# Kernel optimization log

Hardware: AMD Instinct MI355X
Metric: run time of the kernel (lower is better)

The kernel has to match this reference:

```python
import jax, jax.numpy as jnp
import numpy as np

N = 50000          # nodes
E = 800000         # edges (before self loops)
F_IN = 16
HID = 64
HEADS = 4
C = 64             # per-head out channels (concat=False)
G = 64             # graphs in batch
NEG_SLOPE = 0.2


def setup_inputs() -> dict:
    key = jax.random.key(0)
    ks = jax.random.split(key, 20)
    inp = {
        "x": jax.random.normal(ks[0], (N, F_IN), jnp.float32),
        "edge_index": jax.random.randint(ks[1], (2, E), 0, N, jnp.int64),
        "batch": jnp.sort(jax.random.randint(ks[2], (N,), 0, G, jnp.int64)),
        "W_in": jax.random.normal(ks[3], (HID, F_IN), jnp.float32) * 0.1,
        "b_in": jnp.zeros((HID,), jnp.float32),
        "W_out": jax.random.normal(ks[4], (1, HID), jnp.float32) * 0.1,
        "b_out": jnp.zeros((1,), jnp.float32),
    }
    for l in range(3):
        inp[f"W{l}"] = jax.random.normal(ks[5 + 4 * l], (HEADS * C, HID), jnp.float32) * 0.1
        inp[f"asrc{l}"] = jax.random.normal(ks[6 + 4 * l], (HEADS, C), jnp.float32) * 0.1
        inp[f"adst{l}"] = jax.random.normal(ks[7 + 4 * l], (HEADS, C), jnp.float32) * 0.1
        inp[f"bg{l}"] = jnp.zeros((HID,), jnp.float32)
    return inp


def _gat_layer(x, W, a_src, a_dst, bias, src, dst, n):
    # x: [N, HID] -> h: [N, HEADS, C]
    h = (x @ W.T).reshape(n, HEADS, C)
    alpha_s = jnp.einsum("nhc,hc->nh", h, a_src)   # [N, H]
    alpha_d = jnp.einsum("nhc,hc->nh", h, a_dst)
    e = jax.nn.leaky_relu(alpha_s[src] + alpha_d[dst], NEG_SLOPE)  # [E', H]
    # segment softmax over incoming edges of each dst node
    m = jax.ops.segment_max(e, dst, num_segments=n)
    e = jnp.exp(e - m[dst])
    s = jax.ops.segment_sum(e, dst, num_segments=n)
    alpha = e / (s[dst] + 1e-16)                                   # [E', H]
    msg = alpha[:, :, None] * h[src]                               # [E', H, C]
    out = jax.ops.segment_sum(msg, dst, num_segments=n)            # [N, H, C]
    return out.mean(axis=1) + bias                                 # concat=False: head mean


def reference(x, W_in, b_in, W0, asrc0, adst0, bg0, W1, asrc1, adst1, bg1,
              W2, asrc2, adst2, bg2, W_out, b_out, edge_index, batch):
    n = x.shape[0]
    # add self loops (PyG GATConv default)
    loops = jnp.arange(n, dtype=edge_index.dtype)
    src = jnp.concatenate([edge_index[0], loops])
    dst = jnp.concatenate([edge_index[1], loops])

    h = x @ W_in.T + b_in
    for W, a_s, a_d, bg in ((W0, asrc0, adst0, bg0),
                            (W1, asrc1, adst1, bg1),
                            (W2, asrc2, adst2, bg2)):
        h = jax.nn.relu(_gat_layer(h, W, a_s, a_d, bg, src, dst, n))
        # dropout p=0.2 is inactive in eval mode

    # global mean pool over graphs
    sums = jax.ops.segment_sum(h, batch, num_segments=G)
    cnt = jax.ops.segment_sum(jnp.ones((n,), h.dtype), batch, num_segments=G)
    graph_emb = sums / jnp.maximum(cnt, 1.0)[:, None]              # [G, HID]

    return jax.nn.sigmoid(graph_emb @ W_out.T + b_out)             # [G, 1]
```

## Files before the change

### kernel.cpp

```cpp
#include <hip/hip_runtime.h>
#include <hip/hip_bf16.h>
#include <hip/hip_fp16.h>

#define HID 64
#define HEADS 4
#define GCNT 64
#define F_IN 16
#define NEG 0.2f
#define NBUCK 256
#define BSLOT 6144
#define SCHUNK 2048

typedef _Float16 f16x8 __attribute__((ext_vector_type(8)));
typedef float f32x4 __attribute__((ext_vector_type(4)));

__device__ __forceinline__ unsigned pack_h2(float a, float b) {
  __half2 h = __floats2half2_rn(a, b);
  union { __half2 h; unsigned u; } c;
  c.h = h;
  return c.u;
}
__device__ __forceinline__ __half2 uas_h2(unsigned u) {
  union { unsigned u; __half2 h; } c;
  c.u = u;
  return c.h;
}
__device__ __forceinline__ unsigned h2_as_u(__half2 h) {
  union { __half2 h; unsigned u; } c;
  c.h = h;
  return c.u;
}
__device__ __forceinline__ __half2 xor16_add(__half2 v) {
  unsigned u = (unsigned)__shfl_xor((int)h2_as_u(v), 16, 64);
  return __hadd2(v, uas_h2(u));
}

__global__ __launch_bounds__(256) void k_pre(
    const float* __restrict__ W0, const float* __restrict__ asrc,
    const float* __restrict__ adst, const float* __restrict__ Win,
    const float* __restrict__ bin, int* __restrict__ bcur,
    float* __restrict__ vb, float* __restrict__ c8) {
  int t = threadIdx.x;
  if (blockIdx.x == 0) {
    bcur[t] = 0;
    return;
  }
  __shared__ float vaL[512];
#pragma unroll
  for (int it = 0; it < 2; ++it) {
    int idx = t + it * 256;
    int q = idx >> 6, j = idx & 63;
    const float* a = (q < 4) ? asrc : adst;
    int h = q & 3;
    float s = 0.f;
    for (int c = 0; c < 64; ++c) s += a[h * 64 + c] * W0[(h * 64 + c) * 64 + j];
    vaL[idx] = s;
  }
  __syncthreads();
  if (t < 128) {
    int q = t >> 4, k = t & 15;
    float s = 0.f;
    for (int j = 0; j < 64; ++j) s += vaL[q * 64 + j] * Win[j * F_IN + k];
    vb[t] = s;
  } else if (t < 136) {
    int q = t - 128;
    float s = 0.f;
    for (int j = 0; j < 64; ++j) s += vaL[q * 64 + j] * bin[j];
    c8[q] = s;
  }
}

__global__ __launch_bounds__(256) void k_bucket(
    const int* __restrict__ ei, int* __restrict__ bcur,
    unsigned* __restrict__ tmp, int E, int N) {
  __shared__ int hist[NBUCK];
  __shared__ int base[NBUCK];
  int t = threadIdx.x;
  int start = blockIdx.x * SCHUNK;
  int end = min(start + SCHUNK, E + N);
  hist[t] = 0;
  __syncthreads();
  unsigned val[8];
  int rank[8];
  bool ok[8];
#pragma unroll
  for (int k = 0; k < 8; ++k) {
    int i = start + t + k * 256;
    ok[k] = i < end;
    if (ok[k]) {
      int s, d;
      if (i < E) {
        s = ei[i];
        d = ei[E + i];
      } else {
        s = d = i - E;
      }
      val[k] = ((unsigned)d << 16) | (unsigned)s;
      rank[k] = atomicAdd(&hist[d >> 8], 1);
    }
  }
  __syncthreads();
  int h = hist[t];
  base[t] = h ? atomicAdd(&bcur[t], h) : 0;
  __syncthreads();
#pragma unroll
  for (int k = 0; k < 8; ++k) {
    if (ok[k]) {
      int bk = (int)(val[k] >> 24);
      int idx = base[bk] + rank[k];
      if (idx < BSLOT) tmp[(size_t)bk * BSLOT + idx] = val[k];
    }
  }
}

__global__ __launch_bounds__(256) void k_bsort(
    const unsigned* __restrict__ tmp, const int* __restrict__ bcur,
    int* __restrict__ rowptr, int* __restrict__ col, int N) {
  __shared__ int s[NBUCK];
  __shared__ int hist[NBUCK];
  __shared__ int pref[NBUCK];
  int b = blockIdx.x, t = threadIdx.x;
  int c = min(bcur[t], BSLOT);
  s[t] = c;
  __syncthreads();
  for (int o = 1; o < 256; o <<= 1) {
    int x = (t >= o) ? s[t - o] : 0;
    __syncthreads();
    s[t] += x;
    __syncthreads();
  }
  int base = (b == 0) ? 0 : s[b - 1];
  int total = s[255];
  int cntb = min(bcur[b], BSLOT);
  hist[t] = 0;
  __syncthreads();
  for (int j = t; j < cntb; j += 256)
    atomicAdd(&hist[(tmp[(size_t)b * BSLOT + j] >> 16) & 255], 1);
  __syncthreads();
  int v = hist[t];
  pref[t] = v;
  __syncthreads();
  for (int o = 1; o < 256; o <<= 1) {
    int x = (t >= o) ? pref[t - o] : 0;
    __syncthreads();
    pref[t] += x;
    __syncthreads();
  }
  pref[t] -= v;
  __syncthreads();
  int node = b * 256 + t;
  if (node < N) rowptr[node] = base + pref[t];
  if (b == 255 && t == 255) rowptr[N] = total;
  hist[t] = 0;
  __syncthreads();
  for (int j = t; j < cntb; j += 256) {
    unsigned e = tmp[(size_t)b * BSLOT + j];
    int d8 = (int)((e >> 16) & 255);
    int r = atomicAdd(&hist[d8], 1);
    col[base + pref[d8] + r] = (int)(e & 0xffffu);
  }
}

__global__ void k_init(const float* __restrict__ x, const float* __restrict__ Win,
                       const float* __restrict__ bin,
                       const float* __restrict__ W0, const float* __restrict__ W1,
                       const float* __restrict__ W2,
                       __half* __restrict__ Wh3, __half* __restrict__ Wcat3,
                       float* __restrict__ sums, const float* __restrict__ vb,
                       const float* __restrict__ c8,
                       float* __restrict__ as_, float* __restrict__ ad_,
                       __half* __restrict__ hh, int N) {
  int b = blockIdx.x, t = threadIdx.x;
  if (b < 384) {
    int i = b * 256 + t;
    if (i < 49152) {
      const float* W = (i < 16384) ? W0 : (i < 32768) ? W1 : W2;
      Wh3[i] = __float2half(W[i & 16383]);
    } else {
      int j = i - 49152;
      int l = j >> 14;
      int r = j & 16383;
      int c = r >> 8;
      int k256 = r & 255;
      int h = k256 & 3, kk = k256 >> 2;
      const float* W = (l == 0) ? W0 : (l == 1) ? W1 : W2;
      Wcat3[j] = __float2half(0.25f * W[(h * 64 + c) * 64 + kk]);
    }
    return;
  }
  if (b < 401) {
    int i = (b - 384) * 256 + t;
    if (i < GCNT * HID + GCNT) sums[i] = 0.f;
    return;
  }
  int i = (b - 401) * 256 + t;
  if (i >= N * HID) return;
  int n = i >> 6, j = i & 63;
  const float* xr = x + (size_t)n * F_IN;
  const float* wr = Win + j * F_IN;
  float xv[F_IN];
  float acc = bin[j];
#pragma unroll
  for (int k = 0; k < F_IN; ++k) {
    xv[k] = xr[k];
    acc = fmaf(xv[k], wr[k], acc);
  }
  hh[i] = __float2half(acc);
  if (j < 8) {
    const float* vbq = vb + j * 16;
    float s = c8[j];
#pragma unroll
    for (int k = 0; k < F_IN; ++k) s = fmaf(xv[k], vbq[k], s);
    if (j < 4) as_[(size_t)n * 4 + j] = s;
    else ad_[(size_t)n * 4 + (j - 4)] = s;
  }
}

__device__ __forceinline__ void gat_one_node(
    int node, int lane, const __half* __restrict__ h, const float* __restrict__ as_,
    const float* __restrict__ ad_, const int* __restrict__ rowptr,
    const int* __restrict__ col, __half* __restrict__ Mrow) {
  int r0 = rowptr[node];
  int deg = rowptr[node + 1] - r0;
  float4 adv = *(const float4*)(ad_ + (size_t)node * 4);

  if (deg <= 64) {
    int off = 0;
    float x0 = 0.f, x1 = 0.f, x2 = 0.f, x3 = 0.f;
    if (lane < deg) {
      int s = col[r0 + lane];
      off = s << 6;
      float4 av = *(const float4*)(as_ + (size_t)s * 4);
      float e0 = av.x + adv.x; e0 = (e0 > 0.f) ? e0 : NEG * e0;
      float e1 = av.y + adv.y; e1 = (e1 > 0.f) ? e1 : NEG * e1;
      float e2 = av.z + adv.z; e2 = (e2 > 0.f) ? e2 : NEG * e2;
      float e3 = av.w + adv.w; e3 = (e3 > 0.f) ? e3 : NEG * e3;
      x0 = __expf(fminf(e0, 60.f));
      x1 = __expf(fminf(e1, 60.f));
      x2 = __expf(fminf(e2, 60.f));
      x3 = __expf(fminf(e3, 60.f));
    }
    float s0 = x0, s1 = x1, s2 = x2, s3 = x3;
#pragma unroll
    for (int o = 32; o; o >>= 1) {
      s0 += __shfl_xor(s0, o, 64);
      s1 += __shfl_xor(s1, o, 64);
      s2 += __shfl_xor(s2, o, 64);
      s3 += __shfl_xor(s3, o, 64);
    }
    unsigned w01 = pack_h2(x0 / (s0 + 1e-16f), x1 / (s1 + 1e-16f));
    unsigned w23 = pack_h2(x2 / (s2 + 1e-16f), x3 / (s3 + 1e-16f));
    __half2 acc01 = __floats2half2_rn(0.f, 0.f);
    __half2 acc23 = acc01;
#pragma unroll 4
    for (int j = 0; j < deg; ++j) {
      int oj = __builtin_amdgcn_readlane(off, j) + lane;
      unsigned W01 = __builtin_amdgcn_readlane(w01, j);
      unsigned W23 = __builtin_amdgcn_readlane(w23, j);
      __half2 hv = __half2half2(h[oj]);
      acc01 = __hfma2(hv, uas_h2(W01), acc01);
      acc23 = __hfma2(hv, uas_h2(W23), acc23);
    }
    *(__half2*)&Mrow[lane * 4] = acc01;
    *(__half2*)&Mrow[lane * 4 + 2] = acc23;
    return;
  }
  float m0 = -1e30f, m1 = -1e30f, m2 = -1e30f, m3 = -1e30f;
  for (int j = lane; j < deg; j += 64) {
    int s = col[r0 + j];
    float4 av = *(const float4*)(as_ + (size_t)s * 4);
    float e0 = av.x + adv.x; e0 = (e0 > 0.f) ? e0 : NEG * e0; m0 = fmaxf(m0, e0);
    float e1 = av.y + adv.y; e1 = (e1 > 0.f) ? e1 : NEG * e1; m1 = fmaxf(m1, e1);
    float e2 = av.z + adv.z; e2 = (e2 > 0.f) ? e2 : NEG * e2; m2 = fmaxf(m2, e2);
    float e3 = av.w + adv.w; e3 = (e3 > 0.f) ? e3 : NEG * e3; m3 = fmaxf(m3, e3);
  }
#pragma unroll
  for (int o = 32; o; o >>= 1) {
    m0 = fmaxf(m0, __shfl_xor(m0, o, 64));
    m1 = fmaxf(m1, __shfl_xor(m1, o, 64));
    m2 = fmaxf(m2, __shfl_xor(m2, o, 64));
    m3 = fmaxf(m3, __shfl_xor(m3, o, 64));
  }
  float s0 = 0.f, s1 = 0.f, s2 = 0.f, s3 = 0.f;
  for (int j = lane; j < deg; j += 64) {
    int s = col[r0 + j];
    float4 av = *(const float4*)(as_ + (size_t)s * 4);
    float e0 = av.x + adv.x; e0 = (e0 > 0.f) ? e0 : NEG * e0; s0 += __expf(e0 - m0);
    float e1 = av.y + adv.y; e1 = (e1 > 0.f) ? e1 : NEG * e1; s1 += __expf(e1 - m1);
    float e2 = av.z + adv.z; e2 = (e2 > 0.f) ? e2 : NEG * e2; s2 += __expf(e2 - m2);
    float e3 = av.w + adv.w; e3 = (e3 > 0.f) ? e3 : NEG * e3; s3 += __expf(e3 - m3);
  }
#pragma unroll
  for (int o = 32; o; o >>= 1) {
    s0 += __shfl_xor(s0, o, 64);
    s1 += __shfl_xor(s1, o, 64);
    s2 += __shfl_xor(s2, o, 64);
    s3 += __shfl_xor(s3, o, 64);
  }
  float i0 = 1.f / (s0 + 1e-16f), i1 = 1.f / (s1 + 1e-16f);
  float i2 = 1.f / (s2 + 1e-16f), i3 = 1.f / (s3 + 1e-16f);
  float a0 = 0.f, a1 = 0.f, a2 = 0.f, a3 = 0.f;
  for (int j = 0; j < deg; ++j) {
    int s = col[r0 + j];
    float4 av = *(const float4*)(as_ + (size_t)s * 4);
    float e0 = av.x + adv.x; e0 = (e0 > 0.f) ? e0 : NEG * e0;
    float e1 = av.y + adv.y; e1 = (e1 > 0.f) ? e1 : NEG * e1;
    float e2 = av.z + adv.z; e2 = (e2 > 0.f) ? e2 : NEG * e2;
    float e3 = av.w + adv.w; e3 = (e3 > 0.f) ? e3 : NEG * e3;
    float hv = __half2float(h[(s << 6) + lane]);
    a0 = fmaf(__expf(e0 - m0) * i0, hv, a0);
    a1 = fmaf(__expf(e1 - m1) * i1, hv, a1);
    a2 = fmaf(__expf(e2 - m2) * i2, hv, a2);
    a3 = fmaf(__expf(e3 - m3) * i3, hv, a3);
  }
  *(__half2*)&Mrow[lane * 4] = __floats2half2_rn(a0, a1);
  *(__half2*)&Mrow[lane * 4 + 2] = __floats2half2_rn(a2, a3);
}

__device__ __forceinline__ void gat_pair(
    int pr, int lane, int half, int l5, int N,
    const __half* __restrict__ h, const float* __restrict__ as_,
    const float* __restrict__ ad_, const int* __restrict__ rowptr,
    const int* __restrict__ col, __half* __restrict__ Mt) {
  int n0 = pr * 2;
  int n1 = min(n0 + 1, N - 1);
  int mynode = half ? n1 : n0;
  int r0 = rowptr[mynode];
  int dg = rowptr[mynode + 1] - r0;
  int dgA = __builtin_amdgcn_readlane(dg, 0);
  int dgB = __builtin_amdgcn_readlane(dg, 32);

  if (dgA <= 32 && dgB <= 32) {
    float4 adv = *(const float4*)(ad_ + (size_t)mynode * 4);
    int off = 0;
    float x0 = 0.f, x1 = 0.f, x2 = 0.f, x3 = 0.f;
    if (l5 < dg) {
      int s = col[r0 + l5];
      off = s << 6;
      float4 av = *(const float4*)(as_ + (size_t)s * 4);
      float e0 = av.x + adv.x; e0 = (e0 > 0.f) ? e0 : NEG * e0;
      float e1 = av.y + adv.y; e1 = (e1 > 0.f) ? e1 : NEG * e1;
      float e2 = av.z + adv.z; e2 = (e2 > 0.f) ? e2 : NEG * e2;
      float e3 = av.w + adv.w; e3 = (e3 > 0.f) ? e3 : NEG * e3;
      x0 = __expf(fminf(e0, 60.f));
      x1 = __expf(fminf(e1, 60.f));
      x2 = __expf(fminf(e2, 60.f));
      x3 = __expf(fminf(e3, 60.f));
    }
    float s0 = x0, s1 = x1, s2 = x2, s3 = x3;
#pragma unroll
    for (int o = 16; o; o >>= 1) {
      s0 += __shfl_xor(s0, o, 64);
      s1 += __shfl_xor(s1, o, 64);
      s2 += __shfl_xor(s2, o, 64);
      s3 += __shfl_xor(s3, o, 64);
    }
    unsigned w01 = pack_h2(x0 / (s0 + 1e-16f), x1 / (s1 + 1e-16f));
    unsigned w23 = pack_h2(x2 / (s2 + 1e-16f), x3 / (s3 + 1e-16f));

    int g = l5 >> 4, li = l5 & 15;
    const uint2* h4p = (const uint2*)h;
    __half2 z = __floats2half2_rn(0.f, 0.f);
    __half2 a0_01 = z, a0_23 = z, a1_01 = z, a1_23 = z;
    __half2 a2_01 = z, a2_23 = z, a3_01 = z, a3_23 = z;
    int mdeg = max(dgA, dgB);
    int baddr = half << 7;
#pragma unroll 2
    for (int j = 0; j < mdeg; j += 2) {
      int addr = baddr + (j + g) * 4;
      int oj = __builtin_amdgcn_ds_bpermute(addr, off);
      unsigned W01 = (unsigned)__builtin_amdgcn_ds_bpermute(addr, (int)w01);
      unsigned W23 = (unsigned)__builtin_amdgcn_ds_bpermute(addr, (int)w23);
      uint2 hv = h4p[(oj >> 2) + li];
      __half2 ha = uas_h2(hv.x), hb = uas_h2(hv.y);
      __half2 wA = uas_h2(W01), wB = uas_h2(W23);
      __half2 c0 = __low2half2(ha), c1 = __high2half2(ha);
      __half2 c2 = __low2half2(hb), c3 = __high2half2(hb);
      a0_01 = __hfma2(c0, wA, a0_01); a0_23 = __hfma2(c0, wB, a0_23);
      a1_01 = __hfma2(c1, wA, a1_01); a1_23 = __hfma2(c1, wB, a1_23);
      a2_01 = __hfma2(c2, wA, a2_01); a2_23 = __hfma2(c2, wB, a2_23);
      a3_01 = __hfma2(c3, wA, a3_01); a3_23 = __hfma2(c3, wB, a3_23);
    }
    a0_01 = xor16_add(a0_01); a0_23 = xor16_add(a0_23);
    a1_01 = xor16_add(a1_01); a1_23 = xor16_add(a1_23);
    a2_01 = xor16_add(a2_01); a2_23 = xor16_add(a2_23);
    a3_01 = xor16_add(a3_01); a3_23 = xor16_add(a3_23);
    if (g == 0) {
      __half* row = &Mt[(mynode & 15) * 264 + li * 16];
      uint4 st1, st2;
      st1.x = h2_as_u(a0_01); st1.y = h2_as_u(a0_23);
      st1.z = h2_as_u(a1_01); st1.w = h2_as_u(a1_23);
      st2.x = h2_as_u(a2_01); st2.y = h2_as_u(a2_23);
      st2.z = h2_as_u(a3_01); st2.w = h2_as_u(a3_23);
      *(uint4*)&row[0] = st1;
      *(uint4*)&row[8] = st2;
    }
  } else {
    gat_one_node(n0, lane, h, as_, ad_, rowptr, col, &Mt[(n0 & 15) * 264]);
    if (n1 != n0) gat_one_node(n1, lane, h, as_, ad_, rowptr, col, &Mt[(n1 & 15) * 264]);
  }
}

template <bool FIN>
__global__ __launch_bounds__(256) void k_gatf(
    const __half* __restrict__ h, const float* __restrict__ as_,
    const float* __restrict__ ad_, const int* __restrict__ rowptr,
    const int* __restrict__ col, const __half* __restrict__ Wcat,
    const float* __restrict__ bg, const __half* __restrict__ Wn,
    const float* __restrict__ asrc, const float* __restrict__ adst,
    __half* __restrict__ hout, float* __restrict__ nas, float* __restrict__ nad,
    const int* __restrict__ batchv, float* __restrict__ gsums,
    int N) {
  __shared__ __half Mt[16 * 264];
  __shared__ __half O[16 * 72];
  int tid = threadIdx.x;
  int lane = tid & 63, wv = tid >> 6;
  int tile = blockIdx.x;
  int half = lane >> 5, l5 = lane & 31;
  int npairs = (N + 1) >> 1;

  int pr0 = tile * 8 + wv * 2;
  int pr1 = pr0 + 1;
  bool has0 = pr0 < npairs, has1 = pr1 < npairs;
  if (has0 && has1) {
    int my0 = min(pr0 * 2 + half, N - 1);
    int my1 = min(pr1 * 2 + half, N - 1);
    int r0a = rowptr[my0];
    int dga = rowptr[my0 + 1] - r0a;
    int r0b = rowptr[my1];
    int dgb = rowptr[my1 + 1] - r0b;
    int dA0 = __builtin_amdgcn_readlane(dga, 0);
    int dB0 = __builtin_amdgcn_readlane(dga, 32);
    int dA1 = __builtin_amdgcn_readlane(dgb, 0);
    int dB1 = __builtin_amdgcn_readlane(dgb, 32);

    if (dA0 <= 32 && dB0 <= 32 && dA1 <= 32 && dB1 <= 32) {
      float4 adva = *(const float4*)(ad_ + (size_t)my0 * 4);
      float4 advb = *(const float4*)(ad_ + (size_t)my1 * 4);
      int offa = 0, offb = 0;
      float xa0 = 0.f, xa1 = 0.f, xa2 = 0.f, xa3 = 0.f;
      float xb0 = 0.f, xb1 = 0.f, xb2 = 0.f, xb3 = 0.f;
      if (l5 < dga) {
        int s = col[r0a + l5];
        offa = s << 6;
        float4 av = *(const float4*)(as_ + (size_t)s * 4);
        float e0 = av.x + adva.x; e0 = (e0 > 0.f) ? e0 : NEG * e0;
        float e1 = av.y + adva.y; e1 = (e1 > 0.f) ? e1 : NEG * e1;
        float e2 = av.z + adva.z; e2 = (e2 > 0.f) ? e2 : NEG * e2;
        float e3 = av.w + adva.w; e3 = (e3 > 0.f) ? e3 : NEG * e3;
        xa0 = __expf(fminf(e0, 60.f));
        xa1 = __expf(fminf(e1, 60.f));
        xa2 = __expf(fminf(e2, 60.f));
        xa3 = __expf(fminf(e3, 60.f));
      }
      if (l5 < dgb) {
        int s = col[r0b + l5];
        offb = s << 6;
        float4 av = *(const float4*)(as_ + (size_t)s * 4);
        float e0 = av.x + advb.x; e0 = (e0 > 0.f) ? e0 : NEG * e0;
        float e1 = av.y + advb.y; e1 = (e1 > 0.f) ? e1 : NEG * e1;
        float e2 = av.z + advb.z; e2 = (e2 > 0.f) ? e2 : NEG * e2;
        float e3 = av.w + advb.w; e3 = (e3 > 0.f) ? e3 : NEG * e3;
        xb0 = __expf(fminf(e0, 60.f));
        xb1 = __expf(fminf(e1, 60.f));
        xb2 = __expf(fminf(e2, 60.f));
        xb3 = __expf(fminf(e3, 60.f));
      }
      float sa0 = xa0, sa1 = xa1, sa2 = xa2, sa3 = xa3;
      float sb0 = xb0, sb1 = xb1, sb2 = xb2, sb3 = xb3;
#pragma unroll
      for (int o = 16; o; o >>= 1) {
        sa0 += __shfl_xor(sa0, o, 64);
        sa1 += __shfl_xor(sa1, o, 64);
        sa2 += __shfl_xor(sa2, o, 64);
        sa3 += __shfl_xor(sa3, o, 64);
        sb0 += __shfl_xor(sb0, o, 64);
        sb1 += __shfl_xor(sb1, o, 64);
        sb2 += __shfl_xor(sb2, o, 64);
        sb3 += __shfl_xor(sb3, o, 64);
      }
      unsigned w01a = pack_h2(xa0 / (sa0 + 1e-16f), xa1 / (sa1 + 1e-16f));
      unsigned w23a = pack_h2(xa2 / (sa2 + 1e-16f), xa3 / (sa3 + 1e-16f));
      unsigned w01b = pack_h2(xb0 / (sb0 + 1e-16f), xb1 / (sb1 + 1e-16f));
      unsigned w23b = pack_h2(xb2 / (sb2 + 1e-16f), xb3 / (sb3 + 1e-16f));

      uint4* EB = (uint4*)&Mt[wv * 1056];
      EB[half * 32 + l5] = make_uint4((unsigned)offa, w01a, w23a, 0u);
      EB[64 + half * 32 + l5] = make_uint4((unsigned)offb, w01b, w23b, 0u);

      int g = l5 >> 4, li = l5 & 15;
      const uint2* h4p = (const uint2*)h;
      __half2 z = __floats2half2_rn(0.f, 0.f);
      __half2 pa0 = z, pa1 = z, pa2 = z, pa3 = z, pa4 = z, pa5 = z, pa6 = z, pa7 = z;
      __half2 pb0 = z, pb1 = z, pb2 = z, pb3 = z, pb4 = z, pb5 = z, pb6 = z, pb7 = z;
      int mm = max(max(dA0, dB0), max(dA1, dB1));
      int ebase = half * 32;
#pragma unroll 2
      for (int j = 0; j < mm; j += 2) {
        uint4 ra = EB[ebase + j + g];
        uint4 rb = EB[64 + ebase + j + g];
        uint2 hva = h4p[((int)ra.x >> 2) + li];
        uint2 hvb = h4p[((int)rb.x >> 2) + li];
        {
          __half2 ha = uas_h2(hva.x), hb = uas_h2(hva.y);
          __half2 wA = uas_h2(ra.y), wB = uas_h2(ra.z);
          __half2 c0 = __low2half2(ha), c1 = __high2half2(ha);
          __half2 c2 = __low2half2(hb), c3 = __high2half2(hb);
          pa0 = __hfma2(c0, wA, pa0); pa1 = __hfma2(c0, wB, pa1);
          pa2 = __hfma2(c1, wA, pa2); pa3 = __hfma2(c1, wB, pa3);
          pa4 = __hfma2(c2, wA, pa4); pa5 = __hfma2(c2, wB, pa5);
          pa6 = __hfma2(c3, wA, pa6); pa7 = __hfma2(c3, wB, pa7);
        }
        {
          __half2 ha = uas_h2(hvb.x), hb = uas_h2(hvb.y);
          __half2 wA = uas_h2(rb.y), wB = uas_h2(rb.z);
          __half2 c0 = __low2half2(ha), c1 = __high2half2(ha);
          __half2 c2 = __low2half2(hb), c3 = __high2half2(hb);
          pb0 = __hfma2(c0, wA, pb0); pb1 = __hfma2(c0, wB, pb1);
          pb2 = __hfma2(c1, wA, pb2); pb3 = __hfma2(c1, wB, pb3);
          pb4 = __hfma2(c2, wA, pb4); pb5 = __hfma2(c2, wB, pb5);
          pb6 = __hfma2(c3, wA, pb6); pb7 = __hfma2(c3, wB, pb7);
        }
      }
      pa0 = xor16_add(pa0); pa1 = xor16_add(pa1); pa2 = xor16_add(pa2); pa3 = xor16_add(pa3);
      pa4 = xor16_add(pa4); pa5 = xor16_add(pa5); pa6 = xor16_add(pa6); pa7 = xor16_add(pa7);
      pb0 = xor16_add(pb0); pb1 = xor16_add(pb1); pb2 = xor16_add(pb2); pb3 = xor16_add(pb3);
      pb4 = xor16_add(pb4); pb5 = xor16_add(pb5); pb6 = xor16_add(pb6); pb7 = xor16_add(pb7);
      if (g == 0) {
        __half* rowA = &Mt[(my0 & 15) * 264 + li * 16];
        __half* rowB = &Mt[(my1 & 15) * 264 + li * 16];
        uint4 s1, s2;
        s1.x = h2_as_u(pa0); s1.y = h2_as_u(pa1); s1.z = h2_as_u(pa2); s1.w = h2_as_u(pa3);
        s2.x = h2_as_u(pa4); s2.y = h2_as_u(pa5); s2.z = h2_as_u(pa6); s2.w = h2_as_u(pa7);
        *(uint4*)&rowA[0] = s1;
        *(uint4*)&rowA[8] = s2;
        s1.x = h2_as_u(pb0); s1.y = h2_as_u(pb1); s1.z = h2_as_u(pb2); s1.w = h2_as_u(pb3);
        s2.x = h2_as_u(pb4); s2.y = h2_as_u(pb5); s2.z = h2_as_u(pb6); s2.w = h2_as_u(pb7);
        *(uint4*)&rowB[0] = s1;
        *(uint4*)&rowB[8] = s2;
      }
    } else {
      gat_pair(pr0, lane, half, l5, N, h, as_, ad_, rowptr, col, Mt);
      gat_pair(pr1, lane, half, l5, N, h, as_, ad_, rowptr, col, Mt);
    }
  } else if (has0) {
    gat_pair(pr0, lane, half, l5, N, h, as_, ad_, rowptr, col, Mt);
  }
  __syncthreads();

  int quad = lane >> 4, n16 = lane & 15;
  const f16x8* WC = (const f16x8*)Wcat;
  int ch1 = wv * 16 + n16;
  float bias1 = bg[ch1];
  f32x4 c1 = {0.f, 0.f, 0.f, 0.f};
#pragma unroll
  for (int i = 0; i < 8; ++i) {
    f16x8 a = *(const f16x8*)&Mt[n16 * 264 + (i * 4 + quad) * 8];
    c1 = __builtin_amdgcn_mfma_f32_16x16x32_f16(a, WC[ch1 * 32 + i * 4 + quad], c1, 0, 0, 0);
  }
#pragma unroll
  for (int r = 0; r < 4; ++r) {
    float v = fmaxf(c1[r] + bias1, 0.f);
    O[(quad * 4 + r) * 72 + ch1] = __float2half(v);
  }
  __syncthreads();

  if (FIN) {
    if (tid < 64) {
      float* cnt_ = gsums + GCNT * HID;
      int c = tid;
      int nmax = min(16, N - tile * 16);
      int curg = -1;
      float acc = 0.f;
      int cacc = 0;
      for (int i = 0; i < nmax; ++i) {
        int gph = batchv[tile * 16 + i];
        float v = __half2float(O[i * 72 + c]);
        if (gph != curg) {
          if (curg >= 0) {
            atomicAdd(&gsums[curg * HID + c], acc);
            if (c == 0) atomicAdd(&cnt_[curg], (float)cacc);
          }
          curg = gph;
          acc = 0.f;
          cacc = 0;
        }
        acc += v;
        ++cacc;
      }
      if (curg >= 0) {
        atomicAdd(&gsums[curg * HID + c], acc);
        if (c == 0) atomicAdd(&cnt_[curg], (float)cacc);
      }
    }
    return;
  }

  {
    int nd = tid >> 4, c0 = (tid & 15) * 4;
    int node = tile * 16 + nd;
    if (node < N) {
      uint2 v = *(const uint2*)&O[nd * 72 + c0];
      *(uint2*)&hout[(size_t)node * 64 + c0] = v;
    }
  }
  {
    const f16x8* WN = (const f16x8*)Wn;
    f16x8 a0 = *(const f16x8*)&O[n16 * 72 + quad * 8];
    f16x8 a1 = *(const f16x8*)&O[n16 * 72 + 32 + quad * 8];
    f32x4 accs[4];
#pragma unroll
    for (int nt = 0; nt < 4; ++nt) {
      int ch = wv * 64 + nt * 16 + n16;
      f32x4 zz = {0.f, 0.f, 0.f, 0.f};
      zz = __builtin_amdgcn_mfma_f32_16x16x32_f16(a0, WN[ch * 8 + quad], zz, 0, 0, 0);
      zz = __builtin_amdgcn_mfma_f32_16x16x32_f16(a1, WN[ch * 8 + 4 + quad], zz, 0, 0, 0);
      accs[nt] = zz;
    }
#pragma unroll
    for (int r = 0; r < 4; ++r) {
      float vs = 0.f, vd = 0.f;
#pragma unroll
      for (int nt = 0; nt < 4; ++nt) {
        int ch = wv * 64 + nt * 16 + n16;
        vs = fmaf(accs[nt][r], asrc[ch], vs);
        vd = fmaf(accs[nt][r], adst[ch], vd);
      }
#pragma unroll
      for (int o = 8; o; o >>= 1) {
        vs += __shfl_xor(vs, o, 64);
        vd += __shfl_xor(vd, o, 64);
      }
      int node = tile * 16 + quad * 4 + r;
      if (n16 == 0 && node < N) {
        nas[(size_t)node * 4 + wv] = vs;
        nad[(size_t)node * 4 + wv] = vd;
      }
    }
  }
}

__global__ void k_out(const float* __restrict__ sums, const float* __restrict__ cnt,
                      const float* __restrict__ Wout, const float* __restrict__ bout,
                      float* __restrict__ out) {
  int g = blockIdx.x, lane = threadIdx.x;
  float cg = fmaxf(cnt[g], 1.f);
  float v = (sums[g * HID + lane] / cg) * Wout[lane];
#pragma unroll
  for (int o = 32; o; o >>= 1) v += __shfl_xor(v, o, 64);
  if (lane == 0) out[g] = 1.f / (1.f + __expf(-v));
}

extern "C" void kernel_launch(void* const* d_in, const int* in_sizes, int n_in,
                              void* d_out, int out_size, void* d_ws, size_t ws_size,
                              hipStream_t stream) {
  const float* x    = (const float*)d_in[0];
  const int*   ei   = (const int*)d_in[1];
  const int*   batch= (const int*)d_in[2];
  const float* Win  = (const float*)d_in[3];
  const float* bin  = (const float*)d_in[4];
  const float* Wout = (const float*)d_in[5];
  const float* bout = (const float*)d_in[6];
  const float* Wl[3]    = {(const float*)d_in[7],  (const float*)d_in[11], (const float*)d_in[15]};
  const float* asrcl[3] = {(const float*)d_in[8],  (const float*)d_in[12], (const float*)d_in[16]};
  const float* adstl[3] = {(const float*)d_in[9],  (const float*)d_in[13], (const float*)d_in[17]};
  const float* bgl[3]   = {(const float*)d_in[10], (const float*)d_in[14], (const float*)d_in[18]};

  int N = in_sizes[2];
  int E = in_sizes[1] / 2;
  int EE = E + N;

  char* p = (char*)d_ws;
  auto alloc = [&](size_t bytes) {
    char* r = p;
    p += (bytes + 255) & ~(size_t)255;
    return r;
  };
  int*      rowptr = (int*)alloc((size_t)(N + 1) * 4);
  int*      col    = (int*)alloc((size_t)EE * 4);
  unsigned* tmp    = (unsigned*)alloc((size_t)NBUCK * BSLOT * 4);
  int*      bcur   = (int*)alloc(NBUCK * 4);
  float*    vb     = (float*)alloc(128 * 4);
  float*    c8     = (float*)alloc(8 * 4);
  __half*   hhA    = (__half*)alloc((size_t)N * HID * 2);
  __half*   hhB    = (__half*)alloc((size_t)N * HID * 2);
  float*    asA    = (float*)alloc((size_t)N * HEADS * 4);
  float*    adA    = (float*)alloc((size_t)N * HEADS * 4);
  float*    asB    = (float*)alloc((size_t)N * HEADS * 4);
  float*    adB    = (float*)alloc((size_t)N * HEADS * 4);
  __half*   Wh3    = (__half*)alloc(3 * 16384 * 2);
  __half*   Wcat3  = (__half*)alloc(3 * 16384 * 2);
  float*    sums   = (float*)alloc((size_t)(GCNT * HID + GCNT) * 4);
  float*    cnt    = sums + GCNT * HID;

  int tiles = (N + 15) / 16;

  k_pre<<<2, 256, 0, stream>>>(Wl[0], asrcl[0], adstl[0], Win, bin, bcur, vb, c8);
  k_bucket<<<(EE + SCHUNK - 1) / SCHUNK, 256, 0, stream>>>(ei, bcur, tmp, E, N);
  k_bsort<<<NBUCK, 256, 0, stream>>>(tmp, bcur, rowptr, col, N);

  k_init<<<401 + (N * HID + 255) / 256, 256, 0, stream>>>(
      x, Win, bin, Wl[0], Wl[1], Wl[2], Wh3, Wcat3, sums, vb, c8, asA, adA, hhA, N);

  k_gatf<false><<<tiles, 256, 0, stream>>>(hhA, asA, adA, rowptr, col,
                                           Wcat3, bgl[0], Wh3 + 16384, asrcl[1], adstl[1],
                                           hhB, asB, adB, nullptr, nullptr, N);
  k_gatf<false><<<tiles, 256, 0, stream>>>(hhB, asB, adB, rowptr, col,
                                           Wcat3 + 16384, bgl[1], Wh3 + 32768, asrcl[2], adstl[2],
                                           hhA, asA, adA, nullptr, nullptr, N);
  k_gatf<true><<<tiles, 256, 0, stream>>>(hhA, asA, adA, rowptr, col,
                                          Wcat3 + 32768, bgl[2], nullptr, nullptr, nullptr,
                                          nullptr, nullptr, nullptr, batch, sums, N);

  k_out<<<GCNT, 64, 0, stream>>>(sums, cnt, Wout, bout, (float*)d_out);
}
```

Before: 314.6 us.

## Split fused GAT layer into gather and GEMM kernels, merge bucket with init

Each fused GAT layer kernel is split in two. A gather/softmax kernel writes the aggregated per-node messages to a global buffer M, and a separate MFMA GEMM kernel reads M back. M shares workspace with the bucket temp buffer. The bucketing kernel and the init kernel are also merged into one launch to cut launch count. The split frees shared memory in the gather kernel, which may raise occupancy, but it adds a global round trip of about 25 MB of f16 per layer and three more launches.

Measured after the change: 365.4 us. 1.16x slower.

```diff
diff --git a/kernel.cpp b/kernel.cpp
--- a/kernel.cpp
+++ b/kernel.cpp
@@ -70,46 +70,102 @@
   }
 }
 
-__global__ __launch_bounds__(256) void k_bucket(
+__global__ __launch_bounds__(256) void k_binit(
     const int* __restrict__ ei, int* __restrict__ bcur,
-    unsigned* __restrict__ tmp, int E, int N) {
-  __shared__ int hist[NBUCK];
-  __shared__ int base[NBUCK];
+    unsigned* __restrict__ tmp, int E, int N,
+    const float* __restrict__ x, const float* __restrict__ Win,
+    const float* __restrict__ bin,
+    const float* __restrict__ W0, const float* __restrict__ W1,
+    const float* __restrict__ W2,
+    __half* __restrict__ Wh3, __half* __restrict__ Wcat3,
+    float* __restrict__ sums, const float* __restrict__ vb,
+    const float* __restrict__ c8,
+    float* __restrict__ as_, float* __restrict__ ad_,
+    __half* __restrict__ hh, int BUK) {
   int t = threadIdx.x;
-  int start = blockIdx.x * SCHUNK;
-  int end = min(start + SCHUNK, E + N);
-  hist[t] = 0;
-  __syncthreads();
-  unsigned val[8];
-  int rank[8];
-  bool ok[8];
-#pragma unroll
-  for (int k = 0; k < 8; ++k) {
-    int i = start + t + k * 256;
-    ok[k] = i < end;
-    if (ok[k]) {
-      int s, d;
-      if (i < E) {
-        s = ei[i];
-        d = ei[E + i];
-      } else {
-        s = d = i - E;
-      }
-      val[k] = ((unsigned)d << 16) | (unsigned)s;
-      rank[k] = atomicAdd(&hist[d >> 8], 1);
-    }
-  }
-  __syncthreads();
-  int h = hist[t];
-  base[t] = h ? atomicAdd(&bcur[t], h) : 0;
-  __syncthreads();
-#pragma unroll
-  for (int k = 0; k < 8; ++k) {
-    if (ok[k]) {
-      int bk = (int)(val[k] >> 24);
-      int idx = base[bk] + rank[k];
-      if (idx < BSLOT) tmp[(size_t)bk * BSLOT + idx] = val[k];
-    }
+  if (blockIdx.x < BUK) {
+    __shared__ int hist[NBUCK];
+    __shared__ int base[NBUCK];
+    int start = blockIdx.x * SCHUNK;
+    int end = min(start + SCHUNK, E + N);
+    hist[t] = 0;
+    __syncthreads();
+    unsigned val[8];
+    int rank[8];
+    bool ok[8];
+#pragma unroll
+    for (int k = 0; k < 8; ++k) {
+      int i = start + t + k * 256;
+      ok[k] = i < end;
+      if (ok[k]) {
+        int s, d;
+        if (i < E) {
+          s = ei[i];
+          d = ei[E + i];
+        } else {
+          s = d = i - E;
+        }
+        val[k] = ((unsigned)d << 16) | (unsigned)s;
+        rank[k] = atomicAdd(&hist[d >> 8], 1);
+      }
+    }
+    __syncthreads();
+    int h = hist[t];
+    base[t] = h ? atomicAdd(&bcur[t], h) : 0;
+    __syncthreads();
+#pragma unroll
+    for (int k = 0; k < 8; ++k) {
+      if (ok[k]) {
+        int bk = (int)(val[k] >> 24);
+        int idx = base[bk] + rank[k];
+        if (idx < BSLOT) tmp[(size_t)bk * BSLOT + idx] = val[k];
+      }
+    }
+    return;
+  }
+  int b = blockIdx.x - BUK;
+  if (b < 384) {
+    int i = b * 256 + t;
+    if (i < 49152) {
+      const float* W = (i < 16384) ? W0 : (i < 32768) ? W1 : W2;
+      Wh3[i] = __float2half(W[i & 16383]);
+    } else {
+      int j = i - 49152;
+      int l = j >> 14;
+      int r = j & 16383;
+      int c = r >> 8;
+      int k256 = r & 255;
+      int h = k256 & 3, kk = k256 >> 2;
+      const float* W = (l == 0) ? W0 : (l == 1) ? W1 : W2;
+      Wcat3[j] = __float2half(0.25f * W[(h * 64 + c) * 64 + kk]);
+    }
+    return;
+  }
+  if (b < 401) {
+    int i = (b - 384) * 256 + t;
+    if (i < GCNT * HID + GCNT) sums[i] = 0.f;
+    return;
+  }
+  int i = (b - 401) * 256 + t;
+  if (i >= N * HID) return;
+  int n = i >> 6, j = i & 63;
+  const float* xr = x + (size_t)n * F_IN;
+  const float* wr = Win + j * F_IN;
+  float xv[F_IN];
+  float acc = bin[j];
+#pragma unroll
+  for (int k = 0; k < F_IN; ++k) {
+    xv[k] = xr[k];
+    acc = fmaf(xv[k], wr[k], acc);
+  }
+  hh[i] = __float2half(acc);
+  if (j < 8) {
+    const float* vbq = vb + j * 16;
+    float s = c8[j];
+#pragma unroll
+    for (int k = 0; k < F_IN; ++k) s = fmaf(xv[k], vbq[k], s);
+    if (j < 4) as_[(size_t)n * 4 + j] = s;
+    else ad_[(size_t)n * 4 + (j - 4)] = s;
   }
 }
 
@@ -161,61 +217,6 @@
   }
 }
 
-__global__ void k_init(const float* __restrict__ x, const float* __restrict__ Win,
-                       const float* __restrict__ bin,
-                       const float* __restrict__ W0, const float* __restrict__ W1,
-                       const float* __restrict__ W2,
-                       __half* __restrict__ Wh3, __half* __restrict__ Wcat3,
-                       float* __restrict__ sums, const float* __restrict__ vb,
-                       const float* __restrict__ c8,
-                       float* __restrict__ as_, float* __restrict__ ad_,
-                       __half* __restrict__ hh, int N) {
-  int b = blockIdx.x, t = threadIdx.x;
-  if (b < 384) {
-    int i = b * 256 + t;
-    if (i < 49152) {
-      const float* W = (i < 16384) ? W0 : (i < 32768) ? W1 : W2;
-      Wh3[i] = __float2half(W[i & 16383]);
-    } else {
-      int j = i - 49152;
-      int l = j >> 14;
-      int r = j & 16383;
-      int c = r >> 8;
-      int k256 = r & 255;
-      int h = k256 & 3, kk = k256 >> 2;
-      const float* W = (l == 0) ? W0 : (l == 1) ? W1 : W2;
-      Wcat3[j] = __float2half(0.25f * W[(h * 64 + c) * 64 + kk]);
-    }
-    return;
-  }
-  if (b < 401) {
-    int i = (b - 384) * 256 + t;
-    if (i < GCNT * HID + GCNT) sums[i] = 0.f;
-    return;
-  }
-  int i = (b - 401) * 256 + t;
-  if (i >= N * HID) return;
-  int n = i >> 6, j = i & 63;
-  const float* xr = x + (size_t)n * F_IN;
-  const float* wr = Win + j * F_IN;
-  float xv[F_IN];
-  float acc = bin[j];
-#pragma unroll
-  for (int k = 0; k < F_IN; ++k) {
-    xv[k] = xr[k];
-    acc = fmaf(xv[k], wr[k], acc);
-  }
-  hh[i] = __float2half(acc);
-  if (j < 8) {
-    const float* vbq = vb + j * 16;
-    float s = c8[j];
-#pragma unroll
-    for (int k = 0; k < F_IN; ++k) s = fmaf(xv[k], vbq[k], s);
-    if (j < 4) as_[(size_t)n * 4 + j] = s;
-    else ad_[(size_t)n * 4 + (j - 4)] = s;
-  }
-}
-
 __device__ __forceinline__ void gat_one_node(
     int node, int lane, const __half* __restrict__ h, const float* __restrict__ as_,
     const float* __restrict__ ad_, const int* __restrict__ rowptr,
@@ -321,7 +322,7 @@
     int pr, int lane, int half, int l5, int N,
     const __half* __restrict__ h, const float* __restrict__ as_,
     const float* __restrict__ ad_, const int* __restrict__ rowptr,
-    const int* __restrict__ col, __half* __restrict__ Mt) {
+    const int* __restrict__ col, __half* __restrict__ M) {
   int n0 = pr * 2;
   int n1 = min(n0 + 1, N - 1);
   int mynode = half ? n1 : n0;
@@ -386,7 +387,7 @@
     a2_01 = xor16_add(a2_01); a2_23 = xor16_add(a2_23);
     a3_01 = xor16_add(a3_01); a3_23 = xor16_add(a3_23);
     if (g == 0) {
-      __half* row = &Mt[(mynode & 15) * 264 + li * 16];
+      __half* row = M + (size_t)mynode * 256 + li * 16;
       uint4 st1, st2;
       st1.x = h2_as_u(a0_01); st1.y = h2_as_u(a0_23);
       st1.z = h2_as_u(a1_01); st1.w = h2_as_u(a1_23);
@@ -396,23 +397,16 @@
       *(uint4*)&row[8] = st2;
     }
   } else {
-    gat_one_node(n0, lane, h, as_, ad_, rowptr, col, &Mt[(n0 & 15) * 264]);
-    if (n1 != n0) gat_one_node(n1, lane, h, as_, ad_, rowptr, col, &Mt[(n1 & 15) * 264]);
-  }
-}
-
-template <bool FIN>
-__global__ __launch_bounds__(256) void k_gatf(
+    gat_one_node(n0, lane, h, as_, ad_, rowptr, col, M + (size_t)n0 * 256);
+    if (n1 != n0) gat_one_node(n1, lane, h, as_, ad_, rowptr, col, M + (size_t)n1 * 256);
+  }
+}
+
+__global__ __launch_bounds__(256) void k_gather(
     const __half* __restrict__ h, const float* __restrict__ as_,
     const float* __restrict__ ad_, const int* __restrict__ rowptr,
-    const int* __restrict__ col, const __half* __restrict__ Wcat,
-    const float* __restrict__ bg, const __half* __restrict__ Wn,
-    const float* __restrict__ asrc, const float* __restrict__ adst,
-    __half* __restrict__ hout, float* __restrict__ nas, float* __restrict__ nad,
-    const int* __restrict__ batchv, float* __restrict__ gsums,
-    int N) {
-  __shared__ __half Mt[16 * 264];
-  __shared__ __half O[16 * 72];
+    const int* __restrict__ col, __half* __restrict__ M, int N) {
+  __shared__ uint4 EBs[4][128];
   int tid = threadIdx.x;
   int lane = tid & 63, wv = tid >> 6;
   int tile = blockIdx.x;
@@ -484,21 +478,23 @@
       unsigned w01b = pack_h2(xb0 / (sb0 + 1e-16f), xb1 / (sb1 + 1e-16f));
       unsigned w23b = pack_h2(xb2 / (sb2 + 1e-16f), xb3 / (sb3 + 1e-16f));
 
-      uint4* EB = (uint4*)&Mt[wv * 1056];
+      uint4* EB = EBs[wv];
       EB[half * 32 + l5] = make_uint4((unsigned)offa, w01a, w23a, 0u);
       EB[64 + half * 32 + l5] = make_uint4((unsigned)offb, w01b, w23b, 0u);
+
+      int mm = max(max(dA0, dB0), max(dA1, dB1));
+      int eA = half * 32;
+      int eB = 64 + eA;
 
       int g = l5 >> 4, li = l5 & 15;
       const uint2* h4p = (const uint2*)h;
       __half2 z = __floats2half2_rn(0.f, 0.f);
       __half2 pa0 = z, pa1 = z, pa2 = z, pa3 = z, pa4 = z, pa5 = z, pa6 = z, pa7 = z;
       __half2 pb0 = z, pb1 = z, pb2 = z, pb3 = z, pb4 = z, pb5 = z, pb6 = z, pb7 = z;
-      int mm = max(max(dA0, dB0), max(dA1, dB1));
-      int ebase = half * 32;
 #pragma unroll 2
       for (int j = 0; j < mm; j += 2) {
-        uint4 ra = EB[ebase + j + g];
-        uint4 rb = EB[64 + ebase + j + g];
+        uint4 ra = EB[eA + j + g];
+        uint4 rb = EB[eB + j + g];
         uint2 hva = h4p[((int)ra.x >> 2) + li];
         uint2 hvb = h4p[((int)rb.x >> 2) + li];
         {
@@ -527,8 +523,8 @@
       pb0 = xor16_add(pb0); pb1 = xor16_add(pb1); pb2 = xor16_add(pb2); pb3 = xor16_add(pb3);
       pb4 = xor16_add(pb4); pb5 = xor16_add(pb5); pb6 = xor16_add(pb6); pb7 = xor16_add(pb7);
       if (g == 0) {
-        __half* rowA = &Mt[(my0 & 15) * 264 + li * 16];
-        __half* rowB = &Mt[(my1 & 15) * 264 + li * 16];
+        __half* rowA = M + (size_t)my0 * 256 + li * 16;
+        __half* rowB = M + (size_t)my1 * 256 + li * 16;
         uint4 s1, s2;
         s1.x = h2_as_u(pa0); s1.y = h2_as_u(pa1); s1.z = h2_as_u(pa2); s1.w = h2_as_u(pa3);
         s2.x = h2_as_u(pa4); s2.y = h2_as_u(pa5); s2.z = h2_as_u(pa6); s2.w = h2_as_u(pa7);
@@ -540,22 +536,34 @@
         *(uint4*)&rowB[8] = s2;
       }
     } else {
-      gat_pair(pr0, lane, half, l5, N, h, as_, ad_, rowptr, col, Mt);
-      gat_pair(pr1, lane, half, l5, N, h, as_, ad_, rowptr, col, Mt);
+      gat_pair(pr0, lane, half, l5, N, h, as_, ad_, rowptr, col, M);
+      gat_pair(pr1, lane, half, l5, N, h, as_, ad_, rowptr, col, M);
     }
   } else if (has0) {
-    gat_pair(pr0, lane, half, l5, N, h, as_, ad_, rowptr, col, Mt);
-  }
-  __syncthreads();
-
+    gat_pair(pr0, lane, half, l5, N, h, as_, ad_, rowptr, col, M);
+  }
+}
+
+template <bool FIN>
+__global__ __launch_bounds__(256) void k_gemm(
+    const __half* __restrict__ M, const __half* __restrict__ Wcat,
+    const float* __restrict__ bg, const __half* __restrict__ Wn,
+    const float* __restrict__ asrc, const float* __restrict__ adst,
+    __half* __restrict__ hout, float* __restrict__ nas, float* __restrict__ nad,
+    const int* __restrict__ batchv, float* __restrict__ gsums, int N) {
+  __shared__ __half O[16 * 72];
+  int tid = threadIdx.x;
+  int lane = tid & 63, wv = tid >> 6;
+  int tile = blockIdx.x;
   int quad = lane >> 4, n16 = lane & 15;
   const f16x8* WC = (const f16x8*)Wcat;
   int ch1 = wv * 16 + n16;
   float bias1 = bg[ch1];
   f32x4 c1 = {0.f, 0.f, 0.f, 0.f};
+  const __half* Mrow = M + (size_t)(tile * 16 + n16) * 256;
 #pragma unroll
   for (int i = 0; i < 8; ++i) {
-    f16x8 a = *(const f16x8*)&Mt[n16 * 264 + (i * 4 + quad) * 8];
+    f16x8 a = *(const f16x8*)&Mrow[(i * 4 + quad) * 8];
     c1 = __builtin_amdgcn_mfma_f32_16x16x32_f16(a, WC[ch1 * 32 + i * 4 + quad], c1, 0, 0, 0);
   }
 #pragma unroll
@@ -669,6 +677,7 @@
   int N = in_sizes[2];
   int E = in_sizes[1] / 2;
   int EE = E + N;
+  int tiles = (N + 15) / 16;
 
   char* p = (char*)d_ws;
   auto alloc = [&](size_t bytes) {
@@ -676,9 +685,13 @@
     p += (bytes + 255) & ~(size_t)255;
     return r;
   };
+  size_t msz = (size_t)tiles * 16 * 256 * 2;
+  size_t tsz = (size_t)NBUCK * BSLOT * 4;
+  char*  ov  = alloc(msz > tsz ? msz : tsz);
+  unsigned* tmp = (unsigned*)ov;
+  __half*   M   = (__half*)ov;
   int*      rowptr = (int*)alloc((size_t)(N + 1) * 4);
   int*      col    = (int*)alloc((size_t)EE * 4);
-  unsigned* tmp    = (unsigned*)alloc((size_t)NBUCK * BSLOT * 4);
   int*      bcur   = (int*)alloc(NBUCK * 4);
   float*    vb     = (float*)alloc(128 * 4);
   float*    c8     = (float*)alloc(8 * 4);
@@ -693,23 +706,25 @@
   float*    sums   = (float*)alloc((size_t)(GCNT * HID + GCNT) * 4);
   float*    cnt    = sums + GCNT * HID;
 
-  int tiles = (N + 15) / 16;
+  int BUK = (EE + SCHUNK - 1) / SCHUNK;
+  int initB = 401 + (N * HID + 255) / 256;
 
   k_pre<<<2, 256, 0, stream>>>(Wl[0], asrcl[0], adstl[0], Win, bin, bcur, vb, c8);
-  k_bucket<<<(EE + SCHUNK - 1) / SCHUNK, 256, 0, stream>>>(ei, bcur, tmp, E, N);
+
+  k_binit<<<BUK + initB, 256, 0, stream>>>(ei, bcur, tmp, E, N,
+                                           x, Win, bin, Wl[0], Wl[1], Wl[2],
+                                           Wh3, Wcat3, sums, vb, c8, asA, adA, hhA, BUK);
+
   k_bsort<<<NBUCK, 256, 0, stream>>>(tmp, bcur, rowptr, col, N);
 
-  k_init<<<401 + (N * HID + 255) / 256, 256, 0, stream>>>(
-      x, Win, bin, Wl[0], Wl[1], Wl[2], Wh3, Wcat3, sums, vb, c8, asA, adA, hhA, N);
-
-  k_gatf<false><<<tiles, 256, 0, stream>>>(hhA, asA, adA, rowptr, col,
-                                           Wcat3, bgl[0], Wh3 + 16384, asrcl[1], adstl[1],
+  k_gather<<<tiles, 256, 0, stream>>>(hhA, asA, adA, rowptr, col, M, N);
+  k_gemm<false><<<tiles, 256, 0, stream>>>(M, Wcat3, bgl[0], Wh3 + 16384, asrcl[1], adstl[1],
                                            hhB, asB, adB, nullptr, nullptr, N);
-  k_gatf<false><<<tiles, 256, 0, stream>>>(hhB, asB, adB, rowptr, col,
-                                           Wcat3 + 16384, bgl[1], Wh3 + 32768, asrcl[2], adstl[2],
+  k_gather<<<tiles, 256, 0, stream>>>(hhB, asB, adB, rowptr, col, M, N);
+  k_gemm<false><<<tiles, 256, 0, stream>>>(M, Wcat3 + 16384, bgl[1], Wh3 + 32768, asrcl[2], adstl[2],
                                            hhA, asA, adA, nullptr, nullptr, N);
-  k_gatf<true><<<tiles, 256, 0, stream>>>(hhA, asA, adA, rowptr, col,
-                                          Wcat3 + 32768, bgl[2], nullptr, nullptr, nullptr,
+  k_gather<<<tiles, 256, 0, stream>>>(hhA, asA, adA, rowptr, col, M, N);
+  k_gemm<true><<<tiles, 256, 0, stream>>>(M, Wcat3 + 32768, bgl[2], nullptr, nullptr, nullptr,
                                           nullptr, nullptr, nullptr, batch, sums, N);
 
   k_out<<<GCNT, 64, 0, stream>>>(sums, cnt, Wout, bout, (float*)d_out);
```

## Fuse edge bucketing with init kernel, pad bucket counters, vectorize input projection

Applied to the files above, without the earlier changes.

Merges the edge-bucketing pass and the init kernel into one launch, with block ranges selecting the role, which removes a kernel launch and lets the two independent jobs overlap. The global bucket counters are padded with a stride of 16 so that each atomic counter sits on its own cache line. The input projection now has 4 threads per node working from weights staged in shared memory, each producing 16 outputs with vectorized loads and stores. The cost is higher register and LDS use in the merged kernel, which may lower occupancy for the bucketing blocks.

After: 295.7 us. -6.0%, faster.

```diff
diff --git a/kernel.cpp b/kernel.cpp
--- a/kernel.cpp
+++ b/kernel.cpp
@@ -10,6 +10,7 @@
 #define NBUCK 256
 #define BSLOT 6144
 #define SCHUNK 2048
+#define BSTRIDE 16
 
 typedef _Float16 f16x8 __attribute__((ext_vector_type(8)));
 typedef float f32x4 __attribute__((ext_vector_type(4)));
@@ -42,7 +43,7 @@
     float* __restrict__ vb, float* __restrict__ c8) {
   int t = threadIdx.x;
   if (blockIdx.x == 0) {
-    bcur[t] = 0;
+    for (int i = t; i < NBUCK * BSTRIDE; i += 256) bcur[i] = 0;
     return;
   }
   __shared__ float vaL[512];
@@ -70,107 +71,60 @@
   }
 }
 
-__global__ __launch_bounds__(256) void k_bucket(
+__global__ __launch_bounds__(256) void k_binit(
     const int* __restrict__ ei, int* __restrict__ bcur,
-    unsigned* __restrict__ tmp, int E, int N) {
-  __shared__ int hist[NBUCK];
-  __shared__ int base[NBUCK];
+    unsigned* __restrict__ tmp, int E, int N,
+    const float* __restrict__ x, const float* __restrict__ Win,
+    const float* __restrict__ bin,
+    const float* __restrict__ W0, const float* __restrict__ W1,
+    const float* __restrict__ W2,
+    __half* __restrict__ Wh3, __half* __restrict__ Wcat3,
+    float* __restrict__ sums, const float* __restrict__ vb,
+    const float* __restrict__ c8,
+    float* __restrict__ as_, float* __restrict__ ad_,
+    __half* __restrict__ hh, int BUK) {
   int t = threadIdx.x;
-  int start = blockIdx.x * SCHUNK;
-  int end = min(start + SCHUNK, E + N);
-  hist[t] = 0;
-  __syncthreads();
-  unsigned val[8];
-  int rank[8];
-  bool ok[8];
-#pragma unroll
-  for (int k = 0; k < 8; ++k) {
-    int i = start + t + k * 256;
-    ok[k] = i < end;
-    if (ok[k]) {
-      int s, d;
-      if (i < E) {
-        s = ei[i];
-        d = ei[E + i];
-      } else {
-        s = d = i - E;
-      }
-      val[k] = ((unsigned)d << 16) | (unsigned)s;
-      rank[k] = atomicAdd(&hist[d >> 8], 1);
-    }
-  }
-  __syncthreads();
-  int h = hist[t];
-  base[t] = h ? atomicAdd(&bcur[t], h) : 0;
-  __syncthreads();
-#pragma unroll
-  for (int k = 0; k < 8; ++k) {
-    if (ok[k]) {
-      int bk = (int)(val[k] >> 24);
-      int idx = base[bk] + rank[k];
-      if (idx < BSLOT) tmp[(size_t)bk * BSLOT + idx] = val[k];
-    }
-  }
-}
-
-__global__ __launch_bounds__(256) void k_bsort(
-    const unsigned* __restrict__ tmp, const int* __restrict__ bcur,
-    int* __restrict__ rowptr, int* __restrict__ col, int N) {
-  __shared__ int s[NBUCK];
-  __shared__ int hist[NBUCK];
-  __shared__ int pref[NBUCK];
-  int b = blockIdx.x, t = threadIdx.x;
-  int c = min(bcur[t], BSLOT);
-  s[t] = c;
-  __syncthreads();
-  for (int o = 1; o < 256; o <<= 1) {
-    int x = (t >= o) ? s[t - o] : 0;
+  if (blockIdx.x < BUK) {
+    __shared__ int hist[NBUCK];
+    __shared__ int base[NBUCK];
+    int start = blockIdx.x * SCHUNK;
+    int end = min(start + SCHUNK, E + N);
+    hist[t] = 0;
     __syncthreads();
-    s[t] += x;
+    unsigned val[8];
+    int rank[8];
+    bool ok[8];
+#pragma unroll
+    for (int k = 0; k < 8; ++k) {
+      int i = start + t + k * 256;
+      ok[k] = i < end;
+      if (ok[k]) {
+        int s, d;
+        if (i < E) {
+          s = ei[i];
+          d = ei[E + i];
+        } else {
+          s = d = i - E;
+        }
+        val[k] = ((unsigned)d << 16) | (unsigned)s;
+        rank[k] = atomicAdd(&hist[d >> 8], 1);
+      }
+    }
     __syncthreads();
-  }
-  int base = (b == 0) ? 0 : s[b - 1];
-  int total = s[255];
-  int cntb = min(bcur[b], BSLOT);
-  hist[t] = 0;
-  __syncthreads();
-  for (int j = t; j < cntb; j += 256)
-    atomicAdd(&hist[(tmp[(size_t)b * BSLOT + j] >> 16) & 255], 1);
-  __syncthreads();
-  int v = hist[t];
-  pref[t] = v;
-  __syncthreads();
-  for (int o = 1; o < 256; o <<= 1) {
-    int x = (t >= o) ? pref[t - o] : 0;
+    int h = hist[t];
+    base[t] = h ? atomicAdd(&bcur[t * BSTRIDE], h) : 0;
     __syncthreads();
-    pref[t] += x;
-    __syncthreads();
-  }
-  pref[t] -= v;
-  __syncthreads();
-  int node = b * 256 + t;
-  if (node < N) rowptr[node] = base + pref[t];
-  if (b == 255 && t == 255) rowptr[N] = total;
-  hist[t] = 0;
-  __syncthreads();
-  for (int j = t; j < cntb; j += 256) {
-    unsigned e = tmp[(size_t)b * BSLOT + j];
-    int d8 = (int)((e >> 16) & 255);
-    int r = atomicAdd(&hist[d8], 1);
-    col[base + pref[d8] + r] = (int)(e & 0xffffu);
-  }
-}
-
-__global__ void k_init(const float* __restrict__ x, const float* __restrict__ Win,
-                       const float* __restrict__ bin,
-                       const float* __restrict__ W0, const float* __restrict__ W1,
-                       const float* __restrict__ W2,
-                       __half* __restrict__ Wh3, __half* __restrict__ Wcat3,
-                       float* __restrict__ sums, const float* __restrict__ vb,
-                       const float* __restrict__ c8,
-                       float* __restrict__ as_, float* __restrict__ ad_,
-                       __half* __restrict__ hh, int N) {
-  int b = blockIdx.x, t = threadIdx.x;
+#pragma unroll
+    for (int k = 0; k < 8; ++k) {
+      if (ok[k]) {
+        int bk = (int)(val[k] >> 24);
+        int idx = base[bk] + rank[k];
+        if (idx < BSLOT) tmp[(size_t)bk * BSLOT + idx] = val[k];
+      }
+    }
+    return;
+  }
+  int b = blockIdx.x - BUK;
   if (b < 384) {
     int i = b * 256 + t;
     if (i < 49152) {
@@ -193,26 +147,99 @@
     if (i < GCNT * HID + GCNT) sums[i] = 0.f;
     return;
   }
-  int i = (b - 401) * 256 + t;
-  if (i >= N * HID) return;
-  int n = i >> 6, j = i & 63;
-  const float* xr = x + (size_t)n * F_IN;
-  const float* wr = Win + j * F_IN;
-  float xv[F_IN];
-  float acc = bin[j];
-#pragma unroll
-  for (int k = 0; k < F_IN; ++k) {
-    xv[k] = xr[k];
-    acc = fmaf(xv[k], wr[k], acc);
-  }
-  hh[i] = __float2half(acc);
-  if (j < 8) {
-    const float* vbq = vb + j * 16;
-    float s = c8[j];
-#pragma unroll
-    for (int k = 0; k < F_IN; ++k) s = fmaf(xv[k], vbq[k], s);
-    if (j < 4) as_[(size_t)n * 4 + j] = s;
-    else ad_[(size_t)n * 4 + (j - 4)] = s;
+  {
+    __shared__ float Ws[1024];
+    __shared__ float vbs[128];
+    __shared__ float bins[64];
+    __shared__ float c8s[8];
+    for (int i = t; i < 1024; i += 256) Ws[i] = Win[i];
+    if (t < 128) vbs[t] = vb[t];
+    if (t < 64) bins[t] = bin[t];
+    if (t < 8) c8s[t] = c8[t];
+    __syncthreads();
+    int b2 = b - 401;
+    int n = b2 * 64 + (t >> 2);
+    int p = t & 3;
+    if (n >= N) return;
+    const float4* xr4 = (const float4*)(x + (size_t)n * F_IN);
+    float4 a0 = xr4[0], a1 = xr4[1], a2 = xr4[2], a3 = xr4[3];
+    float xv[16] = {a0.x, a0.y, a0.z, a0.w, a1.x, a1.y, a1.z, a1.w,
+                    a2.x, a2.y, a2.z, a2.w, a3.x, a3.y, a3.z, a3.w};
+    unsigned hv[8];
+#pragma unroll
+    for (int jj = 0; jj < 16; jj += 2) {
+      int j = p * 16 + jj;
+      float acc0 = bins[j], acc1 = bins[j + 1];
+#pragma unroll
+      for (int k = 0; k < 16; ++k) {
+        acc0 = fmaf(xv[k], Ws[j * 16 + k], acc0);
+        acc1 = fmaf(xv[k], Ws[(j + 1) * 16 + k], acc1);
+      }
+      hv[jj >> 1] = pack_h2(acc0, acc1);
+    }
+    uint4* dst = (uint4*)(hh + (size_t)n * 64 + p * 16);
+    dst[0] = make_uint4(hv[0], hv[1], hv[2], hv[3]);
+    dst[1] = make_uint4(hv[4], hv[5], hv[6], hv[7]);
+    if (p == 0) {
+      float sq[8];
+#pragma unroll
+      for (int q = 0; q < 8; ++q) {
+        float s = c8s[q];
+#pragma unroll
+        for (int k = 0; k < 16; ++k) s = fmaf(xv[k], vbs[q * 16 + k], s);
+        sq[q] = s;
+      }
+      *(float4*)(as_ + (size_t)n * 4) = make_float4(sq[0], sq[1], sq[2], sq[3]);
+      *(float4*)(ad_ + (size_t)n * 4) = make_float4(sq[4], sq[5], sq[6], sq[7]);
+    }
+  }
+}
+
+__global__ __launch_bounds__(256) void k_bsort(
+    const unsigned* __restrict__ tmp, const int* __restrict__ bcur,
+    int* __restrict__ rowptr, int* __restrict__ col, int N) {
+  __shared__ int s[NBUCK];
+  __shared__ int hist[NBUCK];
+  __shared__ int pref[NBUCK];
+  int b = blockIdx.x, t = threadIdx.x;
+  int c = min(bcur[t * BSTRIDE], BSLOT);
+  s[t] = c;
+  __syncthreads();
+  for (int o = 1; o < 256; o <<= 1) {
+    int x = (t >= o) ? s[t - o] : 0;
+    __syncthreads();
+    s[t] += x;
+    __syncthreads();
+  }
+  int base = (b == 0) ? 0 : s[b - 1];
+  int total = s[255];
+  int cntb = min(bcur[b * BSTRIDE], BSLOT);
+  hist[t] = 0;
+  __syncthreads();
+  for (int j = t; j < cntb; j += 256)
+    atomicAdd(&hist[(tmp[(size_t)b * BSLOT + j] >> 16) & 255], 1);
+  __syncthreads();
+  int v = hist[t];
+  pref[t] = v;
+  __syncthreads();
+  for (int o = 1; o < 256; o <<= 1) {
+    int x = (t >= o) ? pref[t - o] : 0;
+    __syncthreads();
+    pref[t] += x;
+    __syncthreads();
+  }
+  pref[t] -= v;
+  __syncthreads();
+  int node = b * 256 + t;
+  if (node < N) rowptr[node] = base + pref[t];
+  if (b == 255 && t == 255) rowptr[N] = total;
+  hist[t] = 0;
+  __syncthreads();
+  for (int j = t; j < cntb; j += 256) {
+    unsigned e = tmp[(size_t)b * BSLOT + j];
+    int d8 = (int)((e >> 16) & 255);
+    int r = atomicAdd(&hist[d8], 1);
+    col[base + pref[d8] + r] = (int)(e & 0xffffu);
   }
 }
 
@@ -679,7 +706,7 @@
   int*      rowptr = (int*)alloc((size_t)(N + 1) * 4);
   int*      col    = (int*)alloc((size_t)EE * 4);
   unsigned* tmp    = (unsigned*)alloc((size_t)NBUCK * BSLOT * 4);
-  int*      bcur   = (int*)alloc(NBUCK * 4);
+  int*      bcur   = (int*)alloc((size_t)NBUCK * BSTRIDE * 4);
   float*    vb     = (float*)alloc(128 * 4);
   float*    c8     = (float*)alloc(8 * 4);
   __half*   hhA    = (__half*)alloc((size_t)N * HID * 2);
@@ -694,13 +721,16 @@
   float*    cnt    = sums + GCNT * HID;
 
   int tiles = (N + 15) / 16;
+  int BUK = (EE + SCHUNK - 1) / SCHUNK;
+  int initB = 401 + (N + 63) / 64;
 
   k_pre<<<2, 256, 0, stream>>>(Wl[0], asrcl[0], adstl[0], Win, bin, bcur, vb, c8);
-  k_bucket<<<(EE + SCHUNK - 1) / SCHUNK, 256, 0, stream>>>(ei, bcur, tmp, E, N);
+
+  k_binit<<<BUK + initB, 256, 0, stream>>>(ei, bcur, tmp, E, N,
+                                           x, Win, bin, Wl[0], Wl[1], Wl[2],
+                                           Wh3, Wcat3, sums, vb, c8, asA, adA, hhA, BUK);
+
   k_bsort<<<NBUCK, 256, 0, stream>>>(tmp, bcur, rowptr, col, N);
-
-  k_init<<<401 + (N * HID + 255) / 256, 256, 0, stream>>>(
-      x, Win, bin, Wl[0], Wl[1], Wl[2], Wh3, Wcat3, sums, vb, c8, asA, adA, hhA, N);
 
   k_gatf<false><<<tiles, 256, 0, stream>>>(hhA, asA, adA, rowptr, col,
                                            Wcat3, bgl[0], Wh3 + 16384, asrcl[1], adstl[1],
```
